# Optimization experiments

Hardware: AMD Instinct MI355X
Metric: run time of the kernel (lower is better)

The kernel has to match this reference:

```python
import jax, jax.numpy as jnp
import numpy as np

B, S, H = 1, 2048, 2048
E, K, I = 8, 2, 1024   # n_routed_experts, num_experts_per_tok, moe_intermediate_size
IS = 2 * I             # shared experts intermediate = moe_intermediate_size * n_shared_experts


def setup_inputs() -> dict:
    key = jax.random.key(0)
    ks = jax.random.split(key, 8)
    w = 0.02  # weight scale so gate softmax is not degenerate
    return {
        "x": jax.random.normal(ks[0], (B, S, H), jnp.float32),
        "gate_w": jax.random.normal(ks[1], (E, H), jnp.float32) * w,
        "wg": jax.random.normal(ks[2], (E, H, I), jnp.float32) * w,
        "wu": jax.random.normal(ks[3], (E, H, I), jnp.float32) * w,
        "wd": jax.random.normal(ks[4], (E, I, H), jnp.float32) * w,
        "sg": jax.random.normal(ks[5], (H, IS), jnp.float32) * w,
        "su": jax.random.normal(ks[6], (H, IS), jnp.float32) * w,
        "sd": jax.random.normal(ks[7], (IS, H), jnp.float32) * w,
    }


def reference(x, gate_w, wg, wu, wd, sg, su, sd):
    b, s, h = x.shape
    xf = x.reshape(-1, h)                                  # [T, H]
    T = xf.shape[0]

    # ---- gate: softmax scores, top-k, renormalize ----
    scores = jax.nn.softmax(jnp.einsum("th,eh->te", xf, gate_w), axis=-1)  # [T, E]
    topk_w, topk_i = jax.lax.top_k(scores, K)              # sorted descending
    topk_w = topk_w / jnp.sum(topk_w, axis=-1, keepdims=True)

    # dense combine weights [T, E] (indices unique per token)
    cw = jnp.zeros_like(scores).at[jnp.arange(T)[:, None], topk_i].add(topk_w)

    # ---- routed experts: SwiGLU MLP per expert, weighted combine ----
    g = jnp.einsum("th,ehi->eti", xf, wg)                  # [E, T, I]
    u = jnp.einsum("th,ehi->eti", xf, wu)
    hgated = jax.nn.silu(g) * u
    eo = jnp.einsum("eti,eih->eth", hgated, wd)            # [E, T, H]
    y = jnp.einsum("te,eth->th", cw, eo)                   # [T, H]

    # ---- shared experts ----
    shared = (jax.nn.silu(xf @ sg) * (xf @ su)) @ sd       # [T, H]

    return (y + shared).reshape(b, s, h)
```

## Files before the change

kernel.cpp:

```cpp
#include <hip/hip_runtime.h>


typedef unsigned short u16;
typedef unsigned int   u32;
typedef __bf16 bf16x8 __attribute__((ext_vector_type(8)));
typedef float  f32x4  __attribute__((ext_vector_type(4)));

#define T_TOK 2048
#define HDIM  2048
#define IDIM  1024
#define NEXP  8
#define ISDIM 2048
#define MAXROWS 5120

__device__ __forceinline__ u16 f2bf(float f) {
  u32 x = __float_as_uint(f);
  return (u16)((x + 0x7FFFu + ((x >> 16) & 1u)) >> 16);
}
__device__ __forceinline__ float bf2f(u16 v) { return __uint_as_float(((u32)v) << 16); }

#define GLL(g, l)                                                              \
  __builtin_amdgcn_global_load_lds(                                            \
      (const __attribute__((address_space(1))) void*)(g),                      \
      (__attribute__((address_space(3))) void*)(l), 16, 0, 0)

__global__ void init_kernel(int* __restrict__ perm, int* __restrict__ meta,
                            int* __restrict__ zrow) {
  int idx = blockIdx.x * 256 + threadIdx.x;
  if (idx < 8192) perm[idx] = -1;
  if (idx < 16) meta[idx] = 0;
  if (idx < 1024) zrow[idx] = 0;
}

__global__ __launch_bounds__(256) void gate_kernel(
    const float* __restrict__ x, const float* __restrict__ gw,
    u16* __restrict__ xb, float* __restrict__ outz,
    float* __restrict__ topw, int* __restrict__ topi, int* __restrict__ meta) {
  const int t = blockIdx.x, tid = threadIdx.x;
  const long o = (long)t * HDIM + tid * 8;
  float4 a = *(const float4*)(x + o);
  float4 b = *(const float4*)(x + o + 4);
  float4 z = {0.f, 0.f, 0.f, 0.f};
  *(float4*)(outz + o) = z;
  *(float4*)(outz + o + 4) = z;
  uint4 w;
  w.x = (u32)f2bf(a.x) | ((u32)f2bf(a.y) << 16);
  w.y = (u32)f2bf(a.z) | ((u32)f2bf(a.w) << 16);
  w.z = (u32)f2bf(b.x) | ((u32)f2bf(b.y) << 16);
  w.w = (u32)f2bf(b.z) | ((u32)f2bf(b.w) << 16);
  *(uint4*)(xb + o) = w;
  float acc[NEXP];
#pragma unroll
  for (int e = 0; e < NEXP; e++) {
    const float* gr = gw + e * HDIM + tid * 8;
    float4 wa = *(const float4*)gr;
    float4 wb = *(const float4*)(gr + 4);
    acc[e] = a.x * wa.x + a.y * wa.y + a.z * wa.z + a.w * wa.w +
             b.x * wb.x + b.y * wb.y + b.z * wb.z + b.w * wb.w;
  }
#pragma unroll
  for (int off = 32; off; off >>= 1)
#pragma unroll
    for (int e = 0; e < NEXP; e++) acc[e] += __shfl_down(acc[e], off, 64);
  __shared__ float red[4][NEXP];
  if ((tid & 63) == 0) {
#pragma unroll
    for (int e = 0; e < NEXP; e++) red[tid >> 6][e] = acc[e];
  }
  __syncthreads();
  if (tid == 0) {
    float s[NEXP];
#pragma unroll
    for (int e = 0; e < NEXP; e++) s[e] = red[0][e] + red[1][e] + red[2][e] + red[3][e];
    int i0 = 0;
#pragma unroll
    for (int e = 1; e < NEXP; e++)
      if (s[e] > s[i0]) i0 = e;
    int i1 = -1;
#pragma unroll
    for (int e = 0; e < NEXP; e++) {
      if (e == i0) continue;
      if (i1 < 0 || s[e] > s[i1]) i1 = e;
    }
    float w0 = 1.f / (1.f + __expf(s[i1] - s[i0]));
    topw[t * 2 + 0] = w0;
    topw[t * 2 + 1] = 1.f - w0;
    topi[t * 2 + 0] = i0;
    topi[t * 2 + 1] = i1;
    atomicAdd(meta + i0, 1);
    atomicAdd(meta + i1, 1);
  }
}

__global__ void scan_kernel(int* __restrict__ meta) {
  if (threadIdx.x == 0 && blockIdx.x == 0) {
    int o = 0;
    meta[16] = 0;
#pragma unroll
    for (int e = 0; e < NEXP; e++) {
      o += (meta[e] + 127) & ~127;
      meta[17 + e] = o;
    }
  }
}

__global__ void assign_kernel(const int* __restrict__ topi, int* __restrict__ meta,
                              int* __restrict__ perm, int* __restrict__ tokrow) {
  int idx = blockIdx.x * 256 + threadIdx.x;
  int e = topi[idx];
  int pos = atomicAdd(meta + 8 + e, 1);
  int row = meta[16 + e] + pos;
  perm[row] = idx;
  tokrow[idx] = row;
}

__global__ __launch_bounds__(256) void tcast_kernel(const float* __restrict__ in,
                                                    u16* __restrict__ out, int R, int C,
                                                    long inz, long outz) {
  __shared__ float tile[64 * 65];
  in += (long)blockIdx.z * inz;
  out += (long)blockIdx.z * outz;
  int r0 = blockIdx.y * 64, c0 = blockIdx.x * 64;
  int t = threadIdx.x;
  int i = t >> 4, j4 = t & 15;
#pragma unroll
  for (int ii = 0; ii < 4; ii++) {
    int r = i + ii * 16;
    float4 v = *(const float4*)(in + (long)(r0 + r) * C + c0 + j4 * 4);
    tile[r * 65 + j4 * 4 + 0] = v.x;
    tile[r * 65 + j4 * 4 + 1] = v.y;
    tile[r * 65 + j4 * 4 + 2] = v.z;
    tile[r * 65 + j4 * 4 + 3] = v.w;
  }
  __syncthreads();
  int cc = t >> 3, rr = (t & 7) * 8;
#pragma unroll
  for (int pp = 0; pp < 2; pp++) {
    int c = cc + pp * 32;
    u16 e[8];
#pragma unroll
    for (int u = 0; u < 8; u++) e[u] = f2bf(tile[(rr + u) * 65 + c]);
    uint4 w;
    w.x = (u32)e[0] | ((u32)e[1] << 16);
    w.y = (u32)e[2] | ((u32)e[3] << 16);
    w.z = (u32)e[4] | ((u32)e[5] << 16);
    w.w = (u32)e[6] | ((u32)e[7] << 16);
    *(uint4*)(out + (long)(c0 + c) * R + r0 + rr) = w;
  }
}

template <int HALF8>
__global__ void silu_kernel(u16* __restrict__ buf) {
  long i = (long)blockIdx.x * 256 + threadIdx.x;
  long r = i / HALF8, c = i % HALF8;
  u16* g = buf + r * (long)HALF8 * 16 + c * 8;
  uint4 gv = *(const uint4*)g;
  uint4 uv = *(const uint4*)(g + HALF8 * 8);
  const u32* gp = &gv.x;
  const u32* up = &uv.x;
  uint4 w;
  u32* wp = &w.x;
#pragma unroll
  for (int j = 0; j < 4; j++) {
    float g0 = bf2f((u16)(gp[j] & 0xFFFF)), g1 = bf2f((u16)(gp[j] >> 16));
    float u0 = bf2f((u16)(up[j] & 0xFFFF)), u1 = bf2f((u16)(up[j] >> 16));
    float r0 = g0 / (1.f + __expf(-g0)) * u0;
    float r1 = g1 / (1.f + __expf(-g1)) * u1;
    wp[j] = (u32)f2bf(r0) | ((u32)f2bf(r1) << 16);
  }
  *(uint4*)g = w;
}

template <int CMODE, bool PERMA, bool SEGB>
__device__ __forceinline__ void gemm_body(
    int mt, int nt, u16* ldsA, u16* ldsB, const u16* __restrict__ A, long lda,
    const u16* __restrict__ B, long ldbz, int K, u16* __restrict__ Cb,
    float* __restrict__ Cf, long ldc, const int* __restrict__ offp,
    const int* __restrict__ perm, const float* __restrict__ topw,
    const u16* __restrict__ zrow) {
  const int row0 = mt * 128;
  if constexpr (SEGB) {
    if (row0 >= offp[8]) return;
    int e = 0;
    while (offp[e + 1] <= row0) ++e;
    B += (long)e * ldbz;
  }
  const int tid = threadIdx.x;
  const u16* gA[4];
  const u16* gB[4];
  u16 *lA[4], *lB[4];
#pragma unroll
  for (int j = 0; j < 4; j++) {
    int c = tid + 256 * j;
    int r = c >> 3, s = c & 7;
    int gk = (s ^ (r & 7)) * 8;
    const u16* arow;
    if constexpr (PERMA) {
      int p = perm[row0 + r];
      arow = (p < 0) ? zrow : A + (long)(p >> 1) * lda;
    } else {
      arow = A + (long)(row0 + r) * lda;
    }
    gA[j] = arow + gk;
    gB[j] = B + (long)(nt * 128 + r) * K + gk;
    lA[j] = ldsA + c * 8;
    lB[j] = ldsB + c * 8;
  }
  const int lane = tid & 63, wave = tid >> 6;
  const int wm = (wave & 1) * 64, wn = (wave >> 1) * 64;
  const int lrow = lane & 15;
  const int kchunk = lane >> 4;
  const int rsw = lrow & 7;

  f32x4 acc[4][4];
#pragma unroll
  for (int i = 0; i < 4; i++)
#pragma unroll
    for (int j = 0; j < 4; j++) acc[i][j] = f32x4{0.f, 0.f, 0.f, 0.f};

  const int nk = K >> 6;
  for (int kt = 0; kt < nk; ++kt) {
    const int kk = kt * 64;
#pragma unroll
    for (int j = 0; j < 4; j++) {
      GLL(gA[j] + kk, lA[j]);
      GLL(gB[j] + kk, lB[j]);
    }
    __syncthreads();
#pragma unroll
    for (int half = 0; half < 2; half++) {
      const int slot = (kchunk + half * 4) ^ rsw;
      bf16x8 af[4], bfv[4];
#pragma unroll
      for (int mi = 0; mi < 4; mi++)
        af[mi] = *(const bf16x8*)(ldsA + (wm + lrow + mi * 16) * 64 + slot * 8);
#pragma unroll
      for (int ni = 0; ni < 4; ni++)
        bfv[ni] = *(const bf16x8*)(ldsB + (wn + lrow + ni * 16) * 64 + slot * 8);
#pragma unroll
      for (int mi = 0; mi < 4; mi++)
#pragma unroll
        for (int ni = 0; ni < 4; ni++)
          acc[mi][ni] = __builtin_amdgcn_mfma_f32_16x16x32_bf16(af[mi], bfv[ni],
                                                                acc[mi][ni], 0, 0, 0);
    }
    __syncthreads();
  }

  const int crow = row0 + wm + ((lane >> 4) << 2);
  const int ccol = nt * 128 + wn + (lane & 15);
#pragma unroll
  for (int mi = 0; mi < 4; mi++) {
#pragma unroll
    for (int ni = 0; ni < 4; ni++) {
#pragma unroll
      for (int r = 0; r < 4; r++) {
        int row = crow + mi * 16 + r;
        int col = ccol + ni * 16;
        float v = acc[mi][ni][r];
        if constexpr (CMODE == 0) {
          Cb[(long)row * ldc + col] = f2bf(v);
        } else if constexpr (CMODE == 1) {
          Cf[(long)row * ldc + col] = v;
        } else if constexpr (CMODE == 2) {
          int p = perm[row];
          if (p >= 0) atomicAdd(Cf + (long)(p >> 1) * ldc + col, topw[p] * v);
        } else {
          atomicAdd(Cf + (long)row * ldc + col, v);
        }
      }
    }
  }
}

__global__ __launch_bounds__(256) void gemm_gu_fused(
    const u16* __restrict__ xb, const u16* __restrict__ wguT,
    const u16* __restrict__ sgsuT, u16* __restrict__ gur, u16* __restrict__ gus,
    const int* __restrict__ offp, const int* __restrict__ perm,
    const u16* __restrict__ zrow) {
  __shared__ __align__(16) u16 ldsA[8192], ldsB[8192];
  int bid = blockIdx.x;
  if (bid < 640) {
    gemm_body<0, true, true>(bid / 16, bid % 16, ldsA, ldsB, xb, HDIM, wguT,
                             (long)2 * IDIM * HDIM, HDIM, gur, nullptr, 2 * IDIM, offp,
                             perm, nullptr, zrow);
  } else {
    int b = bid - 640;
    gemm_body<0, false, false>(b / 32, b % 32, ldsA, ldsB, xb, HDIM, sgsuT, 0, HDIM, gus,
                               nullptr, 2 * ISDIM, nullptr, nullptr, nullptr, nullptr);
  }
}

__global__ __launch_bounds__(256) void gemm_down_plain(
    const u16* __restrict__ gus, const u16* __restrict__ sdT,
    const u16* __restrict__ gur, const u16* __restrict__ wdT, float* __restrict__ out,
    u16* __restrict__ eo, const int* __restrict__ offp) {
  __shared__ __align__(16) u16 ldsA[8192], ldsB[8192];
  int bid = blockIdx.x;
  if (bid < 256) {
    gemm_body<1, false, false>(bid / 16, bid % 16, ldsA, ldsB, gus, 2 * ISDIM, sdT, 0,
                               ISDIM, nullptr, out, HDIM, nullptr, nullptr, nullptr,
                               nullptr);
  } else {
    int b = bid - 256;
    gemm_body<0, false, true>(b / 16, b % 16, ldsA, ldsB, gur, 2 * IDIM, wdT,
                              (long)HDIM * IDIM, IDIM, eo, nullptr, HDIM, offp, nullptr,
                              nullptr, nullptr);
  }
}

__global__ __launch_bounds__(256) void combine_kernel(float* __restrict__ out,
                                                      const u16* __restrict__ eo,
                                                      const int* __restrict__ tokrow,
                                                      const float* __restrict__ topw) {
  const int t = blockIdx.x, tid = threadIdx.x;
  const long o = (long)t * HDIM + tid * 8;
  const int r0 = tokrow[t * 2], r1 = tokrow[t * 2 + 1];
  const float w0 = topw[t * 2], w1 = topw[t * 2 + 1];
  float4 a = *(const float4*)(out + o);
  float4 b = *(const float4*)(out + o + 4);
  uint4 e0 = *(const uint4*)(eo + (long)r0 * HDIM + tid * 8);
  uint4 e1 = *(const uint4*)(eo + (long)r1 * HDIM + tid * 8);
  const u32* p0 = &e0.x;
  const u32* p1 = &e1.x;
  float r[8] = {a.x, a.y, a.z, a.w, b.x, b.y, b.z, b.w};
#pragma unroll
  for (int j = 0; j < 4; j++) {
    r[j * 2 + 0] += w0 * bf2f((u16)(p0[j] & 0xFFFF)) + w1 * bf2f((u16)(p1[j] & 0xFFFF));
    r[j * 2 + 1] += w0 * bf2f((u16)(p0[j] >> 16)) + w1 * bf2f((u16)(p1[j] >> 16));
  }
  float4 oa = {r[0], r[1], r[2], r[3]};
  float4 ob = {r[4], r[5], r[6], r[7]};
  *(float4*)(out + o) = oa;
  *(float4*)(out + o + 4) = ob;
}

__global__ __launch_bounds__(256) void gemm_routed_gu(
    const u16* __restrict__ xb, const u16* __restrict__ wT, u16* __restrict__ Cb,
    const int* __restrict__ offp, const int* __restrict__ perm,
    const u16* __restrict__ zrow) {
  __shared__ __align__(16) u16 ldsA[8192], ldsB[8192];
  gemm_body<0, true, true>(blockIdx.y, blockIdx.x, ldsA, ldsB, xb, HDIM, wT,
                           (long)IDIM * HDIM, HDIM, Cb, nullptr, 2 * IDIM, offp, perm,
                           nullptr, zrow);
}
__global__ __launch_bounds__(256) void gemm_shared_gu(const u16* __restrict__ xb,
                                                      const u16* __restrict__ sgsuT,
                                                      u16* __restrict__ gus) {
  __shared__ __align__(16) u16 ldsA[8192], ldsB[8192];
  gemm_body<0, false, false>(blockIdx.y, blockIdx.x, ldsA, ldsB, xb, HDIM, sgsuT, 0, HDIM,
                             gus, nullptr, 2 * ISDIM, nullptr, nullptr, nullptr, nullptr);
}
__global__ __launch_bounds__(256) void gemm_down_atomic(
    const u16* __restrict__ gus, const u16* __restrict__ sdT,
    const u16* __restrict__ gur, const u16* __restrict__ wdT, float* __restrict__ out,
    const int* __restrict__ offp, const int* __restrict__ perm,
    const float* __restrict__ topw) {
  __shared__ __align__(16) u16 ldsA[8192], ldsB[8192];
  int bid = blockIdx.x;
  if (bid < 256) {
    gemm_body<3, false, false>(bid / 16, bid % 16, ldsA, ldsB, gus, 2 * ISDIM, sdT, 0,
                               ISDIM, nullptr, out, HDIM, nullptr, nullptr, nullptr,
                               nullptr);
  } else {
    int b = bid - 256;
    gemm_body<2, false, true>(b / 16, b % 16, ldsA, ldsB, gur, 2 * IDIM, wdT,
                              (long)HDIM * IDIM, IDIM, nullptr, out, HDIM, offp, perm,
                              topw, nullptr);
  }
}

extern "C" void kernel_launch(void* const* d_in, const int* in_sizes, int n_in,
                              void* d_out, int out_size, void* d_ws, size_t ws_size,
                              hipStream_t stream) {
  const float* x  = (const float*)d_in[0];
  const float* gw = (const float*)d_in[1];
  const float* wg = (const float*)d_in[2];
  const float* wu = (const float*)d_in[3];
  const float* wd = (const float*)d_in[4];
  const float* sg = (const float*)d_in[5];
  const float* su = (const float*)d_in[6];
  const float* sd = (const float*)d_in[7];
  float* out = (float*)d_out;

  char* ws = (char*)d_ws;
  size_t off = 0;
  auto alloc = [&](size_t b) {
    size_t o = off;
    off += (b + 255) & ~(size_t)255;
    return (void*)(ws + o);
  };
  u16*   xb     = (u16*)alloc((size_t)T_TOK * HDIM * 2);
  u16*   gur    = (u16*)alloc((size_t)MAXROWS * 2 * IDIM * 2);
  u16*   gus    = (u16*)alloc((size_t)T_TOK * 2 * ISDIM * 2);
  float* topw   = (float*)alloc((size_t)T_TOK * 2 * 4);
  int*   topi   = (int*)alloc((size_t)T_TOK * 2 * 4);
  int*   tokrow = (int*)alloc((size_t)T_TOK * 2 * 4);
  int*   perm   = (int*)alloc(8192 * 4);
  int*   meta   = (int*)alloc(64 * 4);
  u16*   zrow   = (u16*)alloc(4096);
  size_t base = off;

  const size_t SZ_WGUT  = (size_t)NEXP * 2 * IDIM * HDIM * 2;
  const size_t SZ_SGSUT = (size_t)2 * ISDIM * HDIM * 2;
  const size_t SZ_SDT   = (size_t)HDIM * ISDIM * 2;
  const size_t SZ_WDT   = (size_t)NEXP * HDIM * IDIM * 2;
  const bool fused = ws_size >= base + SZ_WGUT + SZ_SGSUT;

  init_kernel<<<32, 256, 0, stream>>>(perm, meta, (int*)zrow);
  gate_kernel<<<T_TOK, 256, 0, stream>>>(x, gw, xb, out, topw, topi, meta);
  scan_kernel<<<1, 64, 0, stream>>>(meta);
  assign_kernel<<<16, 256, 0, stream>>>(topi, meta, perm, tokrow);

  if (fused) {
    u16* wguT  = (u16*)(ws + base);
    u16* sgsuT = (u16*)(ws + base + SZ_WGUT);
    u16* sdT   = wguT;
    u16* wdT   = wguT + SZ_SDT / 2;
    u16* eo    = wguT + (SZ_SDT + SZ_WDT) / 2;
    tcast_kernel<<<dim3(IDIM / 64, HDIM / 64, NEXP), 256, 0, stream>>>(
        wg, wguT, HDIM, IDIM, (long)HDIM * IDIM, (long)2 * IDIM * HDIM);
    tcast_kernel<<<dim3(IDIM / 64, HDIM / 64, NEXP), 256, 0, stream>>>(
        wu, wguT + (size_t)IDIM * HDIM, HDIM, IDIM, (long)HDIM * IDIM,
        (long)2 * IDIM * HDIM);
    tcast_kernel<<<dim3(ISDIM / 64, HDIM / 64, 1), 256, 0, stream>>>(sg, sgsuT, HDIM,
                                                                     ISDIM, 0, 0);
    tcast_kernel<<<dim3(ISDIM / 64, HDIM / 64, 1), 256, 0, stream>>>(
        su, sgsuT + (size_t)ISDIM * HDIM, HDIM, ISDIM, 0, 0);
    gemm_gu_fused<<<1152, 256, 0, stream>>>(xb, wguT, sgsuT, gur, gus, meta + 16, perm,
                                            zrow);
    silu_kernel<128><<<(MAXROWS * IDIM / 8) / 256, 256, 0, stream>>>(gur);
    silu_kernel<256><<<(T_TOK * ISDIM / 8) / 256, 256, 0, stream>>>(gus);
    tcast_kernel<<<dim3(HDIM / 64, ISDIM / 64, 1), 256, 0, stream>>>(sd, sdT, ISDIM,
                                                                     HDIM, 0, 0);
    tcast_kernel<<<dim3(HDIM / 64, IDIM / 64, NEXP), 256, 0, stream>>>(
        wd, wdT, IDIM, HDIM, (long)IDIM * HDIM, (long)HDIM * IDIM);
    gemm_down_plain<<<896, 256, 0, stream>>>(gus, sdT, gur, wdT, out, eo, meta + 16);
    combine_kernel<<<T_TOK, 256, 0, stream>>>(out, eo, tokrow, topw);
  } else {
    u16* wT    = (u16*)(ws + base);
    u16* sgsuT = wT;
    u16* sdT   = wT;
    u16* wdT   = wT + SZ_SDT / 2;
    tcast_kernel<<<dim3(IDIM / 64, HDIM / 64, NEXP), 256, 0, stream>>>(
        wg, wT, HDIM, IDIM, (long)HDIM * IDIM, (long)IDIM * HDIM);
    gemm_routed_gu<<<dim3(8, MAXROWS / 128), 256, 0, stream>>>(xb, wT, gur, meta + 16,
                                                               perm, zrow);
    tcast_kernel<<<dim3(IDIM / 64, HDIM / 64, NEXP), 256, 0, stream>>>(
        wu, wT, HDIM, IDIM, (long)HDIM * IDIM, (long)IDIM * HDIM);
    gemm_routed_gu<<<dim3(8, MAXROWS / 128), 256, 0, stream>>>(xb, wT, gur + IDIM,
                                                               meta + 16, perm, zrow);
    silu_kernel<128><<<(MAXROWS * IDIM / 8) / 256, 256, 0, stream>>>(gur);
    tcast_kernel<<<dim3(ISDIM / 64, HDIM / 64, 1), 256, 0, stream>>>(sg, sgsuT, HDIM,
                                                                     ISDIM, 0, 0);
    tcast_kernel<<<dim3(ISDIM / 64, HDIM / 64, 1), 256, 0, stream>>>(
        su, sgsuT + (size_t)ISDIM * HDIM, HDIM, ISDIM, 0, 0);
    gemm_shared_gu<<<dim3(32, 16), 256, 0, stream>>>(xb, sgsuT, gus);
    silu_kernel<256><<<(T_TOK * ISDIM / 8) / 256, 256, 0, stream>>>(gus);
    tcast_kernel<<<dim3(HDIM / 64, ISDIM / 64, 1), 256, 0, stream>>>(sd, sdT, ISDIM,
                                                                     HDIM, 0, 0);
    tcast_kernel<<<dim3(HDIM / 64, IDIM / 64, NEXP), 256, 0, stream>>>(
        wd, wdT, IDIM, HDIM, (long)IDIM * HDIM, (long)HDIM * IDIM);
    gemm_down_atomic<<<896, 256, 0, stream>>>(gus, sdT, gur, wdT, out, meta + 16, perm,
                                              topw);
  }
}
```

Before: 517.9 us.

## Use 512-thread 128x256 GEMM tiles with triple-buffered LDS and merge small kernels

```diff
diff --git a/kernel.cpp b/kernel.cpp
--- a/kernel.cpp
+++ b/kernel.cpp
@@ -114,12 +114,9 @@
   tokrow[idx] = row;
 }
 
-__global__ __launch_bounds__(256) void tcast_kernel(const float* __restrict__ in,
-                                                    u16* __restrict__ out, int R, int C,
-                                                    long inz, long outz) {
+__device__ __forceinline__ void tcast_tile(const float* __restrict__ in,
+                                           u16* __restrict__ out, int R, int C) {
   __shared__ float tile[64 * 65];
-  in += (long)blockIdx.z * inz;
-  out += (long)blockIdx.z * outz;
   int r0 = blockIdx.y * 64, c0 = blockIdx.x * 64;
   int t = threadIdx.x;
   int i = t >> 4, j4 = t & 15;
@@ -149,9 +146,31 @@
   }
 }
 
+__global__ __launch_bounds__(256) void tcast_kernel(const float* __restrict__ in,
+                                                    u16* __restrict__ out, int R, int C,
+                                                    long inz, long outz) {
+  tcast_tile(in + (long)blockIdx.z * inz, out + (long)blockIdx.z * outz, R, C);
+}
+
+__global__ __launch_bounds__(256) void tcast2_kernel(
+    const float* __restrict__ inA, const float* __restrict__ inB,
+    u16* __restrict__ out, int R, int C, long inz, long outz, long boff, int zsplit) {
+  int z = blockIdx.z;
+  const float* in;
+  u16* o;
+  if (z < zsplit) {
+    in = inA + (long)z * inz;
+    o = out + (long)z * outz;
+  } else {
+    int e = z - zsplit;
+    in = inB + (long)e * inz;
+    o = out + (long)e * outz + boff;
+  }
+  tcast_tile(in, o, R, C);
+}
+
 template <int HALF8>
-__global__ void silu_kernel(u16* __restrict__ buf) {
-  long i = (long)blockIdx.x * 256 + threadIdx.x;
+__device__ __forceinline__ void silu_do(u16* __restrict__ buf, long i) {
   long r = i / HALF8, c = i % HALF8;
   u16* g = buf + r * (long)HALF8 * 16 + c * 8;
   uint4 gv = *(const uint4*)g;
@@ -169,6 +188,194 @@
     wp[j] = (u32)f2bf(r0) | ((u32)f2bf(r1) << 16);
   }
   *(uint4*)g = w;
+}
+
+template <int HALF8>
+__global__ void silu_kernel(u16* __restrict__ buf) {
+  long i = (long)blockIdx.x * 256 + threadIdx.x;
+  silu_do<HALF8>(buf, i);
+}
+
+__global__ void silu2_kernel(u16* __restrict__ gur, u16* __restrict__ gus) {
+  const long NR = (long)MAXROWS * IDIM / 8;
+  long i = (long)blockIdx.x * 256 + threadIdx.x;
+  if (i < NR)
+    silu_do<128>(gur, i);
+  else
+    silu_do<256>(gus, i - NR);
+}
+
+template <int CMODE , bool PERMA, bool SEGB>
+__device__ __forceinline__ void gemm_body2(
+    int mt, int nt, u16* lds, const u16* __restrict__ A, long lda,
+    const u16* __restrict__ B, long ldbz, int K, u16* __restrict__ Cb,
+    float* __restrict__ Cf, long ldc, const int* __restrict__ offp,
+    const int* __restrict__ perm, const u16* __restrict__ zrow) {
+  const int row0 = mt * 128;
+  if constexpr (SEGB) {
+    if (row0 >= offp[8]) return;
+    int e = 0;
+    while (offp[e + 1] <= row0) ++e;
+    B += (long)e * ldbz;
+  }
+  const int tid = threadIdx.x;
+
+  const int ra = tid >> 2, sa = tid & 3;
+  const u16* gA;
+  if constexpr (PERMA) {
+    int p = perm[row0 + ra];
+    gA = ((p < 0) ? zrow : A + (long)(p >> 1) * lda) + (sa ^ ((ra >> 1) & 3)) * 8;
+  } else {
+    gA = A + (long)(row0 + ra) * lda + (sa ^ ((ra >> 1) & 3)) * 8;
+  }
+  const int rb0 = ra, rb1 = ra + 128;
+  const u16* gB0 = B + (long)(nt * 256 + rb0) * K + (sa ^ ((rb0 >> 1) & 3)) * 8;
+  const u16* gB1 = B + (long)(nt * 256 + rb1) * K + (sa ^ ((rb1 >> 1) & 3)) * 8;
+  const int dAo = tid * 8;
+  const int dBo = 4096 + tid * 8;
+
+  const int lane = tid & 63, w = tid >> 6;
+  const int wm = (w >> 2) * 64, wn = (w & 3) * 64;
+  const int lrow = lane & 15, kc = lane >> 4;
+  int offA[4], offB[4];
+#pragma unroll
+  for (int i = 0; i < 4; i++) {
+    int rA = wm + i * 16 + lrow;
+    offA[i] = rA * 32 + (kc ^ ((rA >> 1) & 3)) * 8;
+    int rB = wn + i * 16 + lrow;
+    offB[i] = 4096 + rB * 32 + (kc ^ ((rB >> 1) & 3)) * 8;
+  }
+
+  f32x4 acc[4][4];
+#pragma unroll
+  for (int i = 0; i < 4; i++)
+#pragma unroll
+    for (int j = 0; j < 4; j++) acc[i][j] = f32x4{0.f, 0.f, 0.f, 0.f};
+
+  const int nk = K >> 5;
+  {
+    u16* b0 = lds;
+    GLL(gA, b0 + dAo);
+    GLL(gB0, b0 + dBo);
+    GLL(gB1, b0 + dBo + 4096);
+    u16* b1 = lds + 12288;
+    GLL(gA + 32, b1 + dAo);
+    GLL(gB0 + 32, b1 + dBo);
+    GLL(gB1 + 32, b1 + dBo + 4096);
+  }
+  int cur = 0, stg = 2;
+  for (int t = 0; t < nk; ++t) {
+    asm volatile("s_waitcnt vmcnt(3)" ::: "memory");
+    __builtin_amdgcn_s_barrier();
+    u16* buf = lds + cur * 12288;
+    bf16x8 af[4], bfv[4];
+#pragma unroll
+    for (int i = 0; i < 4; i++) af[i] = *(const bf16x8*)(buf + offA[i]);
+#pragma unroll
+    for (int i = 0; i < 4; i++) bfv[i] = *(const bf16x8*)(buf + offB[i]);
+    int t2 = t + 2;
+    if (t2 >= nk) t2 -= nk;
+    {
+      u16* sb = lds + stg * 12288;
+      const int kk = t2 * 32;
+      GLL(gA + kk, sb + dAo);
+      GLL(gB0 + kk, sb + dBo);
+      GLL(gB1 + kk, sb + dBo + 4096);
+    }
+    __builtin_amdgcn_s_barrier();
+    __builtin_amdgcn_s_setprio(1);
+#pragma unroll
+    for (int mi = 0; mi < 4; mi++)
+#pragma unroll
+      for (int ni = 0; ni < 4; ni++)
+        acc[mi][ni] = __builtin_amdgcn_mfma_f32_16x16x32_bf16(af[mi], bfv[ni],
+                                                              acc[mi][ni], 0, 0, 0);
+    __builtin_amdgcn_s_setprio(0);
+    cur = (cur == 2) ? 0 : cur + 1;
+    stg = (stg == 2) ? 0 : stg + 1;
+  }
+  asm volatile("s_waitcnt vmcnt(0)" ::: "memory");
+
+  const int crow = row0 + wm + ((lane >> 4) << 2);
+  const int ccol = nt * 256 + wn + (lane & 15);
+#pragma unroll
+  for (int mi = 0; mi < 4; mi++) {
+#pragma unroll
+    for (int ni = 0; ni < 4; ni++) {
+#pragma unroll
+      for (int r = 0; r < 4; r++) {
+        int row = crow + mi * 16 + r;
+        int col = ccol + ni * 16;
+        float v = acc[mi][ni][r];
+        if constexpr (CMODE == 0) {
+          Cb[(long)row * ldc + col] = f2bf(v);
+        } else {
+          Cf[(long)row * ldc + col] = v;
+        }
+      }
+    }
+  }
+}
+
+__global__ __launch_bounds__(512, 4) void gemm_gu_fused(
+    const u16* __restrict__ xb, const u16* __restrict__ wguT,
+    const u16* __restrict__ sgsuT, u16* __restrict__ gur, u16* __restrict__ gus,
+    const int* __restrict__ offp, const int* __restrict__ perm,
+    const u16* __restrict__ zrow) {
+  __shared__ __align__(16) u16 lds2[36864];
+  int bid = blockIdx.x;
+  if (bid < 320) {
+    gemm_body2<0, true, true>(bid >> 3, bid & 7, lds2, xb, HDIM, wguT,
+                              (long)2 * IDIM * HDIM, HDIM, gur, nullptr, 2 * IDIM,
+                              offp, perm, zrow);
+  } else {
+    int b = bid - 320;
+    gemm_body2<0, false, false>(b >> 4, b & 15, lds2, xb, HDIM, sgsuT, 0, HDIM, gus,
+                                nullptr, 2 * ISDIM, nullptr, nullptr, nullptr);
+  }
+}
+
+__global__ __launch_bounds__(512, 4) void gemm_down_plain(
+    const u16* __restrict__ gus, const u16* __restrict__ sdT,
+    const u16* __restrict__ gur, const u16* __restrict__ wdT, float* __restrict__ out,
+    u16* __restrict__ eo, const int* __restrict__ offp) {
+  __shared__ __align__(16) u16 lds2[36864];
+  int bid = blockIdx.x;
+  if (bid < 128) {
+    gemm_body2<1, false, false>(bid >> 3, bid & 7, lds2, gus, 2 * ISDIM, sdT, 0, ISDIM,
+                                nullptr, out, HDIM, nullptr, nullptr, nullptr);
+  } else {
+    int b = bid - 128;
+    gemm_body2<0, false, true>(b >> 3, b & 7, lds2, gur, 2 * IDIM, wdT,
+                               (long)HDIM * IDIM, IDIM, eo, nullptr, HDIM, offp,
+                               nullptr, nullptr);
+  }
+}
+
+__global__ __launch_bounds__(256) void combine_kernel(float* __restrict__ out,
+                                                      const u16* __restrict__ eo,
+                                                      const int* __restrict__ tokrow,
+                                                      const float* __restrict__ topw) {
+  const int t = blockIdx.x, tid = threadIdx.x;
+  const long o = (long)t * HDIM + tid * 8;
+  const int r0 = tokrow[t * 2], r1 = tokrow[t * 2 + 1];
+  const float w0 = topw[t * 2], w1 = topw[t * 2 + 1];
+  float4 a = *(const float4*)(out + o);
+  float4 b = *(const float4*)(out + o + 4);
+  uint4 e0 = *(const uint4*)(eo + (long)r0 * HDIM + tid * 8);
+  uint4 e1 = *(const uint4*)(eo + (long)r1 * HDIM + tid * 8);
+  const u32* p0 = &e0.x;
+  const u32* p1 = &e1.x;
+  float r[8] = {a.x, a.y, a.z, a.w, b.x, b.y, b.z, b.w};
+#pragma unroll
+  for (int j = 0; j < 4; j++) {
+    r[j * 2 + 0] += w0 * bf2f((u16)(p0[j] & 0xFFFF)) + w1 * bf2f((u16)(p1[j] & 0xFFFF));
+    r[j * 2 + 1] += w0 * bf2f((u16)(p0[j] >> 16)) + w1 * bf2f((u16)(p1[j] >> 16));
+  }
+  float4 oa = {r[0], r[1], r[2], r[3]};
+  float4 ob = {r[4], r[5], r[6], r[7]};
+  *(float4*)(out + o) = oa;
+  *(float4*)(out + o + 4) = ob;
 }
 
 template <int CMODE, bool PERMA, bool SEGB>
@@ -271,68 +478,6 @@
       }
     }
   }
-}
-
-__global__ __launch_bounds__(256) void gemm_gu_fused(
-    const u16* __restrict__ xb, const u16* __restrict__ wguT,
-    const u16* __restrict__ sgsuT, u16* __restrict__ gur, u16* __restrict__ gus,
-    const int* __restrict__ offp, const int* __restrict__ perm,
-    const u16* __restrict__ zrow) {
-  __shared__ __align__(16) u16 ldsA[8192], ldsB[8192];
-  int bid = blockIdx.x;
-  if (bid < 640) {
-    gemm_body<0, true, true>(bid / 16, bid % 16, ldsA, ldsB, xb, HDIM, wguT,
-                             (long)2 * IDIM * HDIM, HDIM, gur, nullptr, 2 * IDIM, offp,
-                             perm, nullptr, zrow);
-  } else {
-    int b = bid - 640;
-    gemm_body<0, false, false>(b / 32, b % 32, ldsA, ldsB, xb, HDIM, sgsuT, 0, HDIM, gus,
-                               nullptr, 2 * ISDIM, nullptr, nullptr, nullptr, nullptr);
-  }
-}
-
-__global__ __launch_bounds__(256) void gemm_down_plain(
-    const u16* __restrict__ gus, const u16* __restrict__ sdT,
-    const u16* __restrict__ gur, const u16* __restrict__ wdT, float* __restrict__ out,
-    u16* __restrict__ eo, const int* __restrict__ offp) {
-  __shared__ __align__(16) u16 ldsA[8192], ldsB[8192];
-  int bid = blockIdx.x;
-  if (bid < 256) {
-    gemm_body<1, false, false>(bid / 16, bid % 16, ldsA, ldsB, gus, 2 * ISDIM, sdT, 0,
-                               ISDIM, nullptr, out, HDIM, nullptr, nullptr, nullptr,
-                               nullptr);
-  } else {
-    int b = bid - 256;
-    gemm_body<0, false, true>(b / 16, b % 16, ldsA, ldsB, gur, 2 * IDIM, wdT,
-                              (long)HDIM * IDIM, IDIM, eo, nullptr, HDIM, offp, nullptr,
-                              nullptr, nullptr);
-  }
-}
-
-__global__ __launch_bounds__(256) void combine_kernel(float* __restrict__ out,
-                                                      const u16* __restrict__ eo,
-                                                      const int* __restrict__ tokrow,
-                                                      const float* __restrict__ topw) {
-  const int t = blockIdx.x, tid = threadIdx.x;
-  const long o = (long)t * HDIM + tid * 8;
-  const int r0 = tokrow[t * 2], r1 = tokrow[t * 2 + 1];
-  const float w0 = topw[t * 2], w1 = topw[t * 2 + 1];
-  float4 a = *(const float4*)(out + o);
-  float4 b = *(const float4*)(out + o + 4);
-  uint4 e0 = *(const uint4*)(eo + (long)r0 * HDIM + tid * 8);
-  uint4 e1 = *(const uint4*)(eo + (long)r1 * HDIM + tid * 8);
-  const u32* p0 = &e0.x;
-  const u32* p1 = &e1.x;
-  float r[8] = {a.x, a.y, a.z, a.w, b.x, b.y, b.z, b.w};
-#pragma unroll
-  for (int j = 0; j < 4; j++) {
-    r[j * 2 + 0] += w0 * bf2f((u16)(p0[j] & 0xFFFF)) + w1 * bf2f((u16)(p1[j] & 0xFFFF));
-    r[j * 2 + 1] += w0 * bf2f((u16)(p0[j] >> 16)) + w1 * bf2f((u16)(p1[j] >> 16));
-  }
-  float4 oa = {r[0], r[1], r[2], r[3]};
-  float4 ob = {r[4], r[5], r[6], r[7]};
-  *(float4*)(out + o) = oa;
-  *(float4*)(out + o + 4) = ob;
 }
 
 __global__ __launch_bounds__(256) void gemm_routed_gu(
@@ -418,24 +563,20 @@
     u16* sdT   = wguT;
     u16* wdT   = wguT + SZ_SDT / 2;
     u16* eo    = wguT + (SZ_SDT + SZ_WDT) / 2;
-    tcast_kernel<<<dim3(IDIM / 64, HDIM / 64, NEXP), 256, 0, stream>>>(
-        wg, wguT, HDIM, IDIM, (long)HDIM * IDIM, (long)2 * IDIM * HDIM);
-    tcast_kernel<<<dim3(IDIM / 64, HDIM / 64, NEXP), 256, 0, stream>>>(
-        wu, wguT + (size_t)IDIM * HDIM, HDIM, IDIM, (long)HDIM * IDIM,
-        (long)2 * IDIM * HDIM);
-    tcast_kernel<<<dim3(ISDIM / 64, HDIM / 64, 1), 256, 0, stream>>>(sg, sgsuT, HDIM,
-                                                                     ISDIM, 0, 0);
-    tcast_kernel<<<dim3(ISDIM / 64, HDIM / 64, 1), 256, 0, stream>>>(
-        su, sgsuT + (size_t)ISDIM * HDIM, HDIM, ISDIM, 0, 0);
-    gemm_gu_fused<<<1152, 256, 0, stream>>>(xb, wguT, sgsuT, gur, gus, meta + 16, perm,
-                                            zrow);
-    silu_kernel<128><<<(MAXROWS * IDIM / 8) / 256, 256, 0, stream>>>(gur);
-    silu_kernel<256><<<(T_TOK * ISDIM / 8) / 256, 256, 0, stream>>>(gus);
+    tcast2_kernel<<<dim3(IDIM / 64, HDIM / 64, 2 * NEXP), 256, 0, stream>>>(
+        wg, wu, wguT, HDIM, IDIM, (long)HDIM * IDIM, (long)2 * IDIM * HDIM,
+        (long)IDIM * HDIM, NEXP);
+    tcast2_kernel<<<dim3(ISDIM / 64, HDIM / 64, 2), 256, 0, stream>>>(
+        sg, su, sgsuT, HDIM, ISDIM, 0, 0, (long)ISDIM * HDIM, 1);
+    gemm_gu_fused<<<576, 512, 0, stream>>>(xb, wguT, sgsuT, gur, gus, meta + 16, perm,
+                                           zrow);
+    silu2_kernel<<<(MAXROWS * IDIM / 8 + T_TOK * ISDIM / 8) / 256, 256, 0, stream>>>(
+        gur, gus);
     tcast_kernel<<<dim3(HDIM / 64, ISDIM / 64, 1), 256, 0, stream>>>(sd, sdT, ISDIM,
                                                                      HDIM, 0, 0);
     tcast_kernel<<<dim3(HDIM / 64, IDIM / 64, NEXP), 256, 0, stream>>>(
         wd, wdT, IDIM, HDIM, (long)IDIM * HDIM, (long)HDIM * IDIM);
-    gemm_down_plain<<<896, 256, 0, stream>>>(gus, sdT, gur, wdT, out, eo, meta + 16);
+    gemm_down_plain<<<448, 512, 0, stream>>>(gus, sdT, gur, wdT, out, eo, meta + 16);
     combine_kernel<<<T_TOK, 256, 0, stream>>>(out, eo, tokrow, topw);
   } else {
     u16* wT    = (u16*)(ws + base);
```

Result: faster. 498.4 us (-3.8%).
